# Kernel optimization log

Hardware: AMD Instinct MI355X
Metric: run time of the kernel (lower is better)

## Reference

```python
import jax, jax.numpy as jnp
import numpy as np

ALLOWED_SPANLEN = 7
NEG = -10000.0      # init value for logalpha, matching torch fill_(-10000.)
MASK_NEG = -1e9     # additive mask for out-of-window span starts


def setup_inputs() -> dict:
    key = jax.random.key(0)
    k1, k2 = jax.random.split(key)
    B, L, T = 16, 128, 11  # batch, sent_len, tagset_size (9 tags + START + STOP)
    scores = jax.random.normal(k1, (B, L, L, T, T), dtype=jnp.float32)
    # mask holds sentence lengths in [L//2, L] (used as gather index into logalpha)
    mask = jax.random.randint(k2, (B,), L // 2, L + 1, dtype=jnp.int32)
    return {"scores": scores, "mask": mask}


def reference(scores, mask):
    """Semi-CRF forward DP (get_logloss_denominator).

    scores: (B, L, L, T, T) -- scores[b, j, i, y_prev, y] is the score of a span
            [j, i] labeled y, with previous segment label y_prev.
    mask:   (B,) sentence lengths.
    """
    B, L, _, T, _ = scores.shape
    K = ALLOWED_SPANLEN
    start_id, stop_id = T - 1, T - 2

    alpha0 = jnp.full((B, L + 1, T), NEG, dtype=scores.dtype)
    alpha0 = alpha0.at[:, 0, start_id].set(0.0)

    # Re-index scores by span-end position so scan can stream one end per step.
    scores_by_end = jnp.moveaxis(scores, 2, 0)  # (L_end, B, L_start, T, T)
    offs = jnp.arange(K)

    def step(alpha, xs):
        i, sc = xs                # i in [1..L]; sc: (B, L, Tprev, Tcur), end = i-1
        js = i - K + offs         # candidate span starts: [i-K, i-1]
        valid = (js >= 0)[None, :, None, None]
        jsc = jnp.clip(js, 0, L - 1)
        a_w = jnp.take(alpha, jsc, axis=1)   # (B, K, Tprev)
        s_w = jnp.take(sc, jsc, axis=1)      # (B, K, Tprev, Tcur)
        t = jnp.where(valid, s_w + a_w[:, :, :, None], MASK_NEG)
        new = jax.nn.logsumexp(t, axis=(1, 2))           # (B, Tcur)
        alpha = jax.lax.dynamic_update_slice(alpha, new[:, None, :], (0, i, 0))
        return alpha, None

    alpha, _ = jax.lax.scan(step, alpha0, (jnp.arange(1, L + 1), scores_by_end))
    # gather logalpha at the sentence-length position for each batch element
    final = alpha[jnp.arange(B), mask, :]                # (B, T)
    return final[:, stop_id].sum()
```

## Files before the change

### kernel.cpp

```cpp
#include <hip/hip_runtime.h>
#include <math.h>

#define LL 128
#define TT 11
#define NP 121
#define KK 7
#define GS 20
#define SPW 240
#define NSLOT 8
#define PANEF 1024

#define LOG2E 1.4426950408889634f
#define LN2   0.6931471805599453f
#define NEG2  (-10000.0f * LOG2E)
#define MASK2 (-1.0e9f)

typedef const __attribute__((address_space(1))) unsigned int* gas_t;
typedef __attribute__((address_space(3)))       unsigned int* las_t;

__device__ __forceinline__ float fast_exp2(float x) { return __builtin_amdgcn_exp2f(x); }
__device__ __forceinline__ float fast_log2(float x) { return __builtin_amdgcn_logf(x); }
#if __has_builtin(__builtin_amdgcn_rcpf)
__device__ __forceinline__ float fast_rcp(float x) { return __builtin_amdgcn_rcpf(x); }
#else
__device__ __forceinline__ float fast_rcp(float x) { return 1.0f / x; }
#endif
__device__ __forceinline__ float rfl(float x) {
    return __int_as_float(__builtin_amdgcn_readfirstlane(__float_as_int(x)));
}
__device__ __forceinline__ void cfence() { __builtin_amdgcn_wave_barrier(); }
#define VMWAIT20() asm volatile("s_waitcnt vmcnt(20)" ::: "memory")
#define VMWAIT0()  asm volatile("s_waitcnt vmcnt(0)"  ::: "memory")

__global__ __launch_bounds__(256) void hscrf_prep(const float* __restrict__ scores,
                                                  float* __restrict__ E,
                                                  int n_batch)
{
    const int idx = blockIdx.x * blockDim.x + threadIdx.x;
    if (idx >= n_batch * LL * 128) return;
    const int o  = idx & 127;
    const int pi = (idx >> 7) & (LL - 1);
    const int b  = idx >> 14;

    float vals[8];
#pragma unroll
    for (int k = 0; k < 8; ++k) vals[k] = 0.0f;

    if (o < NP) {
        const int y = o / TT, yp = o % TT;
        const float* sb = scores + (size_t)b * (size_t)(LL * LL * NP);
#pragma unroll
        for (int k = 0; k < KK; ++k) {
            const int j = (pi + 1) - KK + k;
            if (j >= 0) {
                const float sc = sb[((size_t)j * LL + pi) * NP + yp * TT + y];
                vals[k] = fast_exp2(sc * LOG2E);
            }
        }
    }
    float4* dst = (float4*)(E + ((size_t)b * LL + pi) * PANEF);
    dst[o]       = make_float4(vals[0], vals[1], vals[2], vals[3]);
    dst[128 + o] = make_float4(vals[4], vals[5], vals[6], vals[7]);
}

__global__ __launch_bounds__(64, 1) void hscrf_dp(const float* __restrict__ E,
                                                  const int* __restrict__ mask,
                                                  float* __restrict__ out,
                                                  int n_batch)
{
    const int l = threadIdx.x;
    const int b = blockIdx.x;
    if (b >= n_batch) return;

    __shared__ __align__(64) float ring[NSLOT][PANEF];
    __shared__ __align__(64) float sp[SPW];

    const int o1  = l + 64;
    const int o1c = (o1 < NP) ? o1 : 0;
    const int y0 = l / TT,   yp0 = l % TT;
    const int y1 = o1c / TT, yp1 = o1c % TT;
    const int i0w = y0 * GS + yp0;
    const int i1w = (o1 < NP) ? (y1 * GS + yp1) : (220 + (l - 57));

    if (l < TT) sp[l * GS + 11] = 0.0f;

    const int mb = mask[b];
    const float* Ebase = E + (size_t)b * (size_t)(LL * PANEF);

    auto dma_pane = [&](int i) {
        const int slot = i & (NSLOT - 1);
        const float* src = Ebase + (size_t)(i - 1) * PANEF;
#pragma unroll
        for (int m = 0; m < 4; ++m)
            __builtin_amdgcn_global_load_lds((gas_t)(src + m * 256 + l * 4),
                                             (las_t)&ring[slot][m * 256], 16, 0, 0);
    };

    float W0[KK], W1[KK];
#pragma unroll
    for (int k = 0; k < KK; ++k) { W0[k] = 0.0f; W1[k] = 0.0f; }
    W0[KK - 1] = (yp0 == TT - 1) ? 1.0f : 0.0f;
    W1[KK - 1] = (yp1 == TT - 1) ? 1.0f : 0.0f;

    float Cc = 0.0f;
    float saved = 0.0f;

    dma_pane(1); dma_pane(2); dma_pane(3);
    dma_pane(4); dma_pane(5); dma_pane(6);
    VMWAIT20();

    const float4* ep1 = (const float4*)&ring[1][0];
    float4 ea0 = ep1[l],      ea1 = ep1[128 + l];
    float4 eb0 = ep1[64 + l], eb1 = ep1[192 + l];

    auto body = [&](int i, bool main) {
        float p0 = fmaf(ea0.x, W0[0], ea0.y * W0[1]);
        float q0 = fmaf(ea0.z, W0[2], ea0.w * W0[3]);
        float u0 = fmaf(ea1.x, W0[4], ea1.y * W0[5]);
        float s0 = (p0 + q0) + fmaf(ea1.z, W0[6], u0);
        float p1 = fmaf(eb0.x, W1[0], eb0.y * W1[1]);
        float q1 = fmaf(eb0.z, W1[2], eb0.w * W1[3]);
        float u1 = fmaf(eb1.x, W1[4], eb1.y * W1[5]);
        float s1 = (p1 + q1) + fmaf(eb1.z, W1[6], u1);
        sp[i0w] = s0;
        sp[i1w] = s1;

        cfence();

        const float4 qa0 = *(const float4*)(sp + yp0 * GS);
        const float4 qb0 = *(const float4*)(sp + yp0 * GS + 4);
        const float4 qc0 = *(const float4*)(sp + yp0 * GS + 8);
        const float4 qa1 = *(const float4*)(sp + yp1 * GS);
        const float4 qb1 = *(const float4*)(sp + yp1 * GS + 4);
        const float4 qc1 = *(const float4*)(sp + yp1 * GS + 8);

        if (main) {
            dma_pane(i + 6);
            VMWAIT20();
        }

        const int ns = (i + 1) & (NSLOT - 1);
        const float4* ep = (const float4*)&ring[ns][0];
        const float4 na0 = ep[l],      na1 = ep[128 + l];
        const float4 nb0 = ep[64 + l], nb1 = ep[192 + l];

        const float SA = (((qa0.x + qa0.y) + (qa0.z + qa0.w)) +
                          ((qb0.x + qb0.y) + (qb0.z + qb0.w))) +
                         ((qc0.x + qc0.y) + (qc0.z + qc0.w));
        const float SB = (((qa1.x + qa1.y) + (qa1.z + qa1.w)) +
                          ((qb1.x + qb1.y) + (qb1.z + qb1.w))) +
                         ((qc1.x + qc1.y) + (qc1.z + qc1.w));

        const float s0u = rfl(SA);
        const float r = fast_rcp(s0u);

        saved = (i == mb) ? Cc + fast_log2(SA) : saved;
        Cc += fast_log2(s0u);

#pragma unroll
        for (int k = 0; k < KK - 1; ++k) { W0[k] = W0[k + 1] * r; W1[k] = W1[k + 1] * r; }
        W0[KK - 1] = SA * r;
        W1[KK - 1] = SB * r;

        ea0 = na0; ea1 = na1; eb0 = nb0; eb1 = nb1;

        cfence();
    };

    for (int i = 1; i <= LL - 6; ++i) body(i, true);
    VMWAIT0();
    for (int i = LL - 5; i <= LL; ++i) body(i, false);

    if (l == TT - 2) {
        atomicAdd(out, saved * LN2);
    }
}

__global__ __launch_bounds__(64, 1) void hscrf_fwd_fb(const float* __restrict__ scores,
                                                      const int* __restrict__ mask,
                                                      float* __restrict__ out,
                                                      int n_batch)
{
    const int l = threadIdx.x;
    const int b = blockIdx.x;
    if (b >= n_batch) return;

    __shared__ __align__(64) float sp[SPW];

    const int o1  = l + 64;
    const int o1c = (o1 < NP) ? o1 : 0;
    const int y0 = l / TT,   yp0 = l % TT;
    const int y1 = o1c / TT, yp1 = o1c % TT;
    const int e0 = yp0 * TT + y0;
    const int e1 = yp1 * TT + y1;
    const int i0w = y0 * GS + yp0;
    const int i1w = (o1 < NP) ? (y1 * GS + yp1) : (220 + (l - 57));

    if (l < TT) sp[l * GS + 11] = 0.0f;

    const int mb = mask[b];
    const float* sb = scores + (size_t)b * (size_t)(LL * LL * NP);

    float win0[KK], win1[KK];
#pragma unroll
    for (int k = 0; k < KK; ++k) { win0[k] = MASK2; win1[k] = MASK2; }
    float na0 = (yp0 == TT - 1) ? 0.0f : NEG2;
    float na1 = (yp1 == TT - 1) ? 0.0f : NEG2;

    float C  = 0.0f, Cn = 0.0f, pp0 = 0.0f, pp1 = 0.0f, saved = 0.0f;

    float cA0[KK], cA1[KK], cB0[KK], cB1[KK];
    float cC0[KK], cC1[KK], cD0[KK], cD1[KK];

    auto load_pane = [&](int i, float (&c0)[KK], float (&c1)[KK]) {
#pragma unroll
        for (int k = 0; k < KK; ++k) {
            int j = i - KK + k;
            int jc = j < 0 ? 0 : j;
            const size_t base = ((size_t)jc * LL + (size_t)(i - 1)) * NP;
            c0[k] = sb[base + e0];
            c1[k] = sb[base + e1];
        }
    };

    load_pane(1, cA0, cA1); load_pane(2, cB0, cB1);
    load_pane(3, cC0, cC1); load_pane(4, cD0, cD1);

    auto step = [&](int i, float (&c0)[KK], float (&c1)[KK],
                    float (&n0)[KK], float (&n1)[KK]) {
#pragma unroll
        for (int k = 0; k < KK - 1; ++k) { win0[k] = win0[k + 1]; win1[k] = win1[k + 1]; }
        win0[KK - 1] = na0;
        win1[KK - 1] = na1;

        const float g0 = fast_exp2(fmaf(c0[KK - 1], LOG2E, win0[KK - 1]) - C);
        const float g1 = fast_exp2(fmaf(c1[KK - 1], LOG2E, win1[KK - 1]) - C);
        sp[i0w] = pp0 + g0;
        sp[i1w] = pp1 + g1;

        if (i + 4 <= LL) load_pane(i + 4, c0, c1);

        cfence();

        const float4 qa0 = *(const float4*)(sp + yp0 * GS);
        const float4 qb0 = *(const float4*)(sp + yp0 * GS + 4);
        const float4 qc0 = *(const float4*)(sp + yp0 * GS + 8);
        const float4 qa1 = *(const float4*)(sp + yp1 * GS);
        const float4 qb1 = *(const float4*)(sp + yp1 * GS + 4);
        const float4 qc1 = *(const float4*)(sp + yp1 * GS + 8);

        float t0 = 0.0f, t1 = 0.0f;
#pragma unroll
        for (int k = 0; k < KK - 1; ++k) {
            t0 += fast_exp2(fmaf(n0[k], LOG2E, win0[k + 1]) - Cn);
            t1 += fast_exp2(fmaf(n1[k], LOG2E, win1[k + 1]) - Cn);
        }
        pp0 = t0; pp1 = t1;

        const float S0 = (((qa0.x + qa0.y) + (qa0.z + qa0.w)) +
                          ((qb0.x + qb0.y) + (qb0.z + qb0.w))) +
                         ((qc0.x + qc0.y) + (qc0.z + qc0.w));
        const float S1 = (((qa1.x + qa1.y) + (qa1.z + qa1.w)) +
                          ((qb1.x + qb1.y) + (qb1.z + qb1.w))) +
                         ((qc1.x + qc1.y) + (qc1.z + qc1.w));

        const float A0 = C + fast_log2(S0);
        const float A1 = C + fast_log2(S1);
        na0 = A0; na1 = A1;
        saved = (i == mb) ? A0 : saved;
        C  = Cn;
        Cn = rfl(A0);

        cfence();
    };

    for (int i = 1; i <= LL; i += 4) {
        step(i,     cA0, cA1, cB0, cB1);
        step(i + 1, cB0, cB1, cC0, cC1);
        step(i + 2, cC0, cC1, cD0, cD1);
        step(i + 3, cD0, cD1, cA0, cA1);
    }

    if (l == TT - 2) atomicAdd(out, saved * LN2);
}

extern "C" void kernel_launch(void* const* d_in, const int* in_sizes, int n_in,
                              void* d_out, int out_size, void* d_ws, size_t ws_size,
                              hipStream_t stream) {
    const float* scores = (const float*)d_in[0];
    const int*   mask   = (const int*)d_in[1];
    float* out = (float*)d_out;
    const int B = in_sizes[1];

    hipMemsetAsync(out, 0, sizeof(float) * out_size, stream);

    const size_t need = (size_t)B * LL * 128 * 8 * sizeof(float);
    if (ws_size >= need) {
        float* E = (float*)d_ws;
        const int total = B * LL * 128;
        hscrf_prep<<<(total + 255) / 256, 256, 0, stream>>>(scores, E, B);
        hscrf_dp<<<B, 64, 0, stream>>>(E, mask, out, B);
    } else {
        hscrf_fwd_fb<<<B, 64, 0, stream>>>(scores, mask, out, B);
    }
}
```

Measured before the change: 210.9 us.

## Fuse exp-prep into DP kernel with register-pipelined raw loads and conversion

```diff
diff --git a/kernel.cpp b/kernel.cpp
--- a/kernel.cpp
+++ b/kernel.cpp
@@ -7,16 +7,9 @@
 #define KK 7
 #define GS 20
 #define SPW 240
-#define NSLOT 8
-#define PANEF 1024
 
 #define LOG2E 1.4426950408889634f
 #define LN2   0.6931471805599453f
-#define NEG2  (-10000.0f * LOG2E)
-#define MASK2 (-1.0e9f)
-
-typedef const __attribute__((address_space(1))) unsigned int* gas_t;
-typedef __attribute__((address_space(3)))       unsigned int* las_t;
 
 __device__ __forceinline__ float fast_exp2(float x) { return __builtin_amdgcn_exp2f(x); }
 __device__ __forceinline__ float fast_log2(float x) { return __builtin_amdgcn_logf(x); }
@@ -29,157 +22,11 @@
     return __int_as_float(__builtin_amdgcn_readfirstlane(__float_as_int(x)));
 }
 __device__ __forceinline__ void cfence() { __builtin_amdgcn_wave_barrier(); }
-#define VMWAIT20() asm volatile("s_waitcnt vmcnt(20)" ::: "memory")
-#define VMWAIT0()  asm volatile("s_waitcnt vmcnt(0)"  ::: "memory")
 
-__global__ __launch_bounds__(256) void hscrf_prep(const float* __restrict__ scores,
-                                                  float* __restrict__ E,
-                                                  int n_batch)
-{
-    const int idx = blockIdx.x * blockDim.x + threadIdx.x;
-    if (idx >= n_batch * LL * 128) return;
-    const int o  = idx & 127;
-    const int pi = (idx >> 7) & (LL - 1);
-    const int b  = idx >> 14;
-
-    float vals[8];
-#pragma unroll
-    for (int k = 0; k < 8; ++k) vals[k] = 0.0f;
-
-    if (o < NP) {
-        const int y = o / TT, yp = o % TT;
-        const float* sb = scores + (size_t)b * (size_t)(LL * LL * NP);
-#pragma unroll
-        for (int k = 0; k < KK; ++k) {
-            const int j = (pi + 1) - KK + k;
-            if (j >= 0) {
-                const float sc = sb[((size_t)j * LL + pi) * NP + yp * TT + y];
-                vals[k] = fast_exp2(sc * LOG2E);
-            }
-        }
-    }
-    float4* dst = (float4*)(E + ((size_t)b * LL + pi) * PANEF);
-    dst[o]       = make_float4(vals[0], vals[1], vals[2], vals[3]);
-    dst[128 + o] = make_float4(vals[4], vals[5], vals[6], vals[7]);
-}
-
-__global__ __launch_bounds__(64, 1) void hscrf_dp(const float* __restrict__ E,
-                                                  const int* __restrict__ mask,
-                                                  float* __restrict__ out,
-                                                  int n_batch)
-{
-    const int l = threadIdx.x;
-    const int b = blockIdx.x;
-    if (b >= n_batch) return;
-
-    __shared__ __align__(64) float ring[NSLOT][PANEF];
-    __shared__ __align__(64) float sp[SPW];
-
-    const int o1  = l + 64;
-    const int o1c = (o1 < NP) ? o1 : 0;
-    const int y0 = l / TT,   yp0 = l % TT;
-    const int y1 = o1c / TT, yp1 = o1c % TT;
-    const int i0w = y0 * GS + yp0;
-    const int i1w = (o1 < NP) ? (y1 * GS + yp1) : (220 + (l - 57));
-
-    if (l < TT) sp[l * GS + 11] = 0.0f;
-
-    const int mb = mask[b];
-    const float* Ebase = E + (size_t)b * (size_t)(LL * PANEF);
-
-    auto dma_pane = [&](int i) {
-        const int slot = i & (NSLOT - 1);
-        const float* src = Ebase + (size_t)(i - 1) * PANEF;
-#pragma unroll
-        for (int m = 0; m < 4; ++m)
-            __builtin_amdgcn_global_load_lds((gas_t)(src + m * 256 + l * 4),
-                                             (las_t)&ring[slot][m * 256], 16, 0, 0);
-    };
-
-    float W0[KK], W1[KK];
-#pragma unroll
-    for (int k = 0; k < KK; ++k) { W0[k] = 0.0f; W1[k] = 0.0f; }
-    W0[KK - 1] = (yp0 == TT - 1) ? 1.0f : 0.0f;
-    W1[KK - 1] = (yp1 == TT - 1) ? 1.0f : 0.0f;
-
-    float Cc = 0.0f;
-    float saved = 0.0f;
-
-    dma_pane(1); dma_pane(2); dma_pane(3);
-    dma_pane(4); dma_pane(5); dma_pane(6);
-    VMWAIT20();
-
-    const float4* ep1 = (const float4*)&ring[1][0];
-    float4 ea0 = ep1[l],      ea1 = ep1[128 + l];
-    float4 eb0 = ep1[64 + l], eb1 = ep1[192 + l];
-
-    auto body = [&](int i, bool main) {
-        float p0 = fmaf(ea0.x, W0[0], ea0.y * W0[1]);
-        float q0 = fmaf(ea0.z, W0[2], ea0.w * W0[3]);
-        float u0 = fmaf(ea1.x, W0[4], ea1.y * W0[5]);
-        float s0 = (p0 + q0) + fmaf(ea1.z, W0[6], u0);
-        float p1 = fmaf(eb0.x, W1[0], eb0.y * W1[1]);
-        float q1 = fmaf(eb0.z, W1[2], eb0.w * W1[3]);
-        float u1 = fmaf(eb1.x, W1[4], eb1.y * W1[5]);
-        float s1 = (p1 + q1) + fmaf(eb1.z, W1[6], u1);
-        sp[i0w] = s0;
-        sp[i1w] = s1;
-
-        cfence();
-
-        const float4 qa0 = *(const float4*)(sp + yp0 * GS);
-        const float4 qb0 = *(const float4*)(sp + yp0 * GS + 4);
-        const float4 qc0 = *(const float4*)(sp + yp0 * GS + 8);
-        const float4 qa1 = *(const float4*)(sp + yp1 * GS);
-        const float4 qb1 = *(const float4*)(sp + yp1 * GS + 4);
-        const float4 qc1 = *(const float4*)(sp + yp1 * GS + 8);
-
-        if (main) {
-            dma_pane(i + 6);
-            VMWAIT20();
-        }
-
-        const int ns = (i + 1) & (NSLOT - 1);
-        const float4* ep = (const float4*)&ring[ns][0];
-        const float4 na0 = ep[l],      na1 = ep[128 + l];
-        const float4 nb0 = ep[64 + l], nb1 = ep[192 + l];
-
-        const float SA = (((qa0.x + qa0.y) + (qa0.z + qa0.w)) +
-                          ((qb0.x + qb0.y) + (qb0.z + qb0.w))) +
-                         ((qc0.x + qc0.y) + (qc0.z + qc0.w));
-        const float SB = (((qa1.x + qa1.y) + (qa1.z + qa1.w)) +
-                          ((qb1.x + qb1.y) + (qb1.z + qb1.w))) +
-                         ((qc1.x + qc1.y) + (qc1.z + qc1.w));
-
-        const float s0u = rfl(SA);
-        const float r = fast_rcp(s0u);
-
-        saved = (i == mb) ? Cc + fast_log2(SA) : saved;
-        Cc += fast_log2(s0u);
-
-#pragma unroll
-        for (int k = 0; k < KK - 1; ++k) { W0[k] = W0[k + 1] * r; W1[k] = W1[k + 1] * r; }
-        W0[KK - 1] = SA * r;
-        W1[KK - 1] = SB * r;
-
-        ea0 = na0; ea1 = na1; eb0 = nb0; eb1 = nb1;
-
-        cfence();
-    };
-
-    for (int i = 1; i <= LL - 6; ++i) body(i, true);
-    VMWAIT0();
-    for (int i = LL - 5; i <= LL; ++i) body(i, false);
-
-    if (l == TT - 2) {
-        atomicAdd(out, saved * LN2);
-    }
-}
-
-__global__ __launch_bounds__(64, 1) void hscrf_fwd_fb(const float* __restrict__ scores,
-                                                      const int* __restrict__ mask,
-                                                      float* __restrict__ out,
-                                                      int n_batch)
+__global__ __launch_bounds__(64, 1) void hscrf_fused(const float* __restrict__ scores,
+                                                     const int* __restrict__ mask,
+                                                     float* __restrict__ out,
+                                                     int n_batch)
 {
     const int l = threadIdx.x;
     const int b = blockIdx.x;
@@ -201,44 +48,61 @@
     const int mb = mask[b];
     const float* sb = scores + (size_t)b * (size_t)(LL * LL * NP);
 
-    float win0[KK], win1[KK];
-#pragma unroll
-    for (int k = 0; k < KK; ++k) { win0[k] = MASK2; win1[k] = MASK2; }
-    float na0 = (yp0 == TT - 1) ? 0.0f : NEG2;
-    float na1 = (yp1 == TT - 1) ? 0.0f : NEG2;
+    float rA0[KK], rA1[KK], rB0[KK], rB1[KK];
+    float rC0[KK], rC1[KK], rD0[KK], rD1[KK];
+    float eX0[KK], eX1[KK], eY0[KK], eY1[KK];
 
-    float C  = 0.0f, Cn = 0.0f, pp0 = 0.0f, pp1 = 0.0f, saved = 0.0f;
-
-    float cA0[KK], cA1[KK], cB0[KK], cB1[KK];
-    float cC0[KK], cC1[KK], cD0[KK], cD1[KK];
-
-    auto load_pane = [&](int i, float (&c0)[KK], float (&c1)[KK]) {
+    auto load_pane = [&](int p, float (&L0)[KK], float (&L1)[KK]) {
 #pragma unroll
         for (int k = 0; k < KK; ++k) {
-            int j = i - KK + k;
-            int jc = j < 0 ? 0 : j;
-            const size_t base = ((size_t)jc * LL + (size_t)(i - 1)) * NP;
-            c0[k] = sb[base + e0];
-            c1[k] = sb[base + e1];
+            const int j  = p - KK + k;
+            const int jc = j < 0 ? 0 : j;
+            const size_t base = ((size_t)jc * LL + (size_t)(p - 1)) * NP;
+            L0[k] = sb[base + e0];
+            L1[k] = sb[base + e1];
         }
     };
 
-    load_pane(1, cA0, cA1); load_pane(2, cB0, cB1);
-    load_pane(3, cC0, cC1); load_pane(4, cD0, cD1);
+    auto convert = [&](int p, const float (&R0)[KK], const float (&R1)[KK],
+                       float (&D0)[KK], float (&D1)[KK]) {
+#pragma unroll
+        for (int k = 0; k < KK; ++k) {
+            const float ev0 = fast_exp2(R0[k] * LOG2E);
+            const float ev1 = fast_exp2(R1[k] * LOG2E);
+            const bool ok = (p - KK + k) >= 0;
+            D0[k] = ok ? ev0 : 0.0f;
+            D1[k] = ok ? ev1 : 0.0f;
+        }
+    };
 
-    auto step = [&](int i, float (&c0)[KK], float (&c1)[KK],
-                    float (&n0)[KK], float (&n1)[KK]) {
+    float W0[KK], W1[KK];
 #pragma unroll
-        for (int k = 0; k < KK - 1; ++k) { win0[k] = win0[k + 1]; win1[k] = win1[k + 1]; }
-        win0[KK - 1] = na0;
-        win1[KK - 1] = na1;
+    for (int k = 0; k < KK; ++k) { W0[k] = 0.0f; W1[k] = 0.0f; }
+    W0[KK - 1] = (yp0 == TT - 1) ? 1.0f : 0.0f;
+    W1[KK - 1] = (yp1 == TT - 1) ? 1.0f : 0.0f;
 
-        const float g0 = fast_exp2(fmaf(c0[KK - 1], LOG2E, win0[KK - 1]) - C);
-        const float g1 = fast_exp2(fmaf(c1[KK - 1], LOG2E, win1[KK - 1]) - C);
-        sp[i0w] = pp0 + g0;
-        sp[i1w] = pp1 + g1;
+    float Cc = 0.0f;
+    float saved = 0.0f;
 
-        if (i + 4 <= LL) load_pane(i + 4, c0, c1);
+    load_pane(1, rA0, rA1); load_pane(2, rB0, rB1);
+    load_pane(3, rC0, rC1); load_pane(4, rD0, rD1);
+    convert(1, rA0, rA1, eX0, eX1);
+    convert(2, rB0, rB1, eY0, eY1);
+
+    auto body = [&](int i, bool do_load, bool do_conv,
+                    float (&EC0)[KK], float (&EC1)[KK],
+                    float (&LT0)[KK], float (&LT1)[KK],
+                    float (&RS0)[KK], float (&RS1)[KK]) {
+        float p0 = fmaf(EC0[0], W0[0], EC0[1] * W0[1]);
+        float q0 = fmaf(EC0[2], W0[2], EC0[3] * W0[3]);
+        float u0 = fmaf(EC0[4], W0[4], EC0[5] * W0[5]);
+        float s0 = (p0 + q0) + fmaf(EC0[6], W0[6], u0);
+        float p1 = fmaf(EC1[0], W1[0], EC1[1] * W1[1]);
+        float q1 = fmaf(EC1[2], W1[2], EC1[3] * W1[3]);
+        float u1 = fmaf(EC1[4], W1[4], EC1[5] * W1[5]);
+        float s1 = (p1 + q1) + fmaf(EC1[6], W1[6], u1);
+        sp[i0w] = s0;
+        sp[i1w] = s1;
 
         cfence();
 
@@ -249,39 +113,44 @@
         const float4 qb1 = *(const float4*)(sp + yp1 * GS + 4);
         const float4 qc1 = *(const float4*)(sp + yp1 * GS + 8);
 
-        float t0 = 0.0f, t1 = 0.0f;
-#pragma unroll
-        for (int k = 0; k < KK - 1; ++k) {
-            t0 += fast_exp2(fmaf(n0[k], LOG2E, win0[k + 1]) - Cn);
-            t1 += fast_exp2(fmaf(n1[k], LOG2E, win1[k + 1]) - Cn);
-        }
-        pp0 = t0; pp1 = t1;
+        if (do_load) load_pane(i + 4, LT0, LT1);
+        if (do_conv) convert(i + 2, RS0, RS1, EC0, EC1);
 
-        const float S0 = (((qa0.x + qa0.y) + (qa0.z + qa0.w)) +
+        const float SA = (((qa0.x + qa0.y) + (qa0.z + qa0.w)) +
                           ((qb0.x + qb0.y) + (qb0.z + qb0.w))) +
                          ((qc0.x + qc0.y) + (qc0.z + qc0.w));
-        const float S1 = (((qa1.x + qa1.y) + (qa1.z + qa1.w)) +
+        const float SB = (((qa1.x + qa1.y) + (qa1.z + qa1.w)) +
                           ((qb1.x + qb1.y) + (qb1.z + qb1.w))) +
                          ((qc1.x + qc1.y) + (qc1.z + qc1.w));
 
-        const float A0 = C + fast_log2(S0);
-        const float A1 = C + fast_log2(S1);
-        na0 = A0; na1 = A1;
-        saved = (i == mb) ? A0 : saved;
-        C  = Cn;
-        Cn = rfl(A0);
+        const float s0u = rfl(SA);
+        const float r = fast_rcp(s0u);
+
+        saved = (i == mb) ? Cc + fast_log2(SA) : saved;
+        Cc += fast_log2(s0u);
+
+#pragma unroll
+        for (int k = 0; k < KK - 1; ++k) { W0[k] = W0[k + 1] * r; W1[k] = W1[k + 1] * r; }
+        W0[KK - 1] = SA * r;
+        W1[KK - 1] = SB * r;
 
         cfence();
     };
 
-    for (int i = 1; i <= LL; i += 4) {
-        step(i,     cA0, cA1, cB0, cB1);
-        step(i + 1, cB0, cB1, cC0, cC1);
-        step(i + 2, cC0, cC1, cD0, cD1);
-        step(i + 3, cD0, cD1, cA0, cA1);
+    for (int i = 1; i <= LL - 4; i += 4) {
+        body(i,     true, true, eX0, eX1, rA0, rA1, rC0, rC1);
+        body(i + 1, true, true, eY0, eY1, rB0, rB1, rD0, rD1);
+        body(i + 2, true, true, eX0, eX1, rC0, rC1, rA0, rA1);
+        body(i + 3, true, true, eY0, eY1, rD0, rD1, rB0, rB1);
     }
+    body(LL - 3, false, true,  eX0, eX1, rA0, rA1, rC0, rC1);
+    body(LL - 2, false, true,  eY0, eY1, rB0, rB1, rD0, rD1);
+    body(LL - 1, false, false, eX0, eX1, rA0, rA1, rA0, rA1);
+    body(LL,     false, false, eY0, eY1, rB0, rB1, rB0, rB1);
 
-    if (l == TT - 2) atomicAdd(out, saved * LN2);
+    if (l == TT - 2) {
+        atomicAdd(out, saved * LN2);
+    }
 }
 
 extern "C" void kernel_launch(void* const* d_in, const int* in_sizes, int n_in,
@@ -294,13 +163,7 @@
 
     hipMemsetAsync(out, 0, sizeof(float) * out_size, stream);
 
-    const size_t need = (size_t)B * LL * 128 * 8 * sizeof(float);
-    if (ws_size >= need) {
-        float* E = (float*)d_ws;
-        const int total = B * LL * 128;
-        hscrf_prep<<<(total + 255) / 256, 256, 0, stream>>>(scores, E, B);
-        hscrf_dp<<<B, 64, 0, stream>>>(E, mask, out, B);
-    } else {
-        hscrf_fwd_fb<<<B, 64, 0, stream>>>(scores, mask, out, B);
-    }
+    (void)d_ws; (void)ws_size;
+
+    hscrf_fused<<<B, 64, 0, stream>>>(scores, mask, out, B);
 }
```

After: 210.4 us. Within noise of the previous version (-0.2%).
